# Kernel optimization log

Hardware: AMD Instinct MI355X
Metric: run time of the kernel (lower is better)

The kernel has to match this reference:

```python
import jax, jax.numpy as jnp
import numpy as np

CONF_THR = 0.01
IOU_THR = 0.45
TOPK = 200
B, N, C = 32, 32768, 81


def centroids2corners(b):
    # (..., 4) cx,cy,w,h -> xmin,ymin,xmax,ymax
    cx, cy, w, h = b[..., 0], b[..., 1], b[..., 2], b[..., 3]
    half_w, half_h = w * 0.5, h * 0.5
    return jnp.stack([cx - half_w, cy - half_h, cx + half_w, cy + half_h], axis=-1)


def iou_matrix(a, b):
    # a: (M,4), b: (N,4) corner format -> (M,N) IoU
    lt = jnp.maximum(a[:, None, :2], b[None, :, :2])
    rb = jnp.minimum(a[:, None, 2:], b[None, :, 2:])
    wh = jnp.clip(rb - lt, 0.0)
    inter = wh[..., 0] * wh[..., 1]
    area_a = (a[:, 2] - a[:, 0]) * (a[:, 3] - a[:, 1])
    area_b = (b[:, 2] - b[:, 0]) * (b[:, 3] - b[:, 1])
    return inter / (area_a[:, None] + area_b[None, :] - inter)


def nms_class(conf_c, loc, c_idx):
    # conf_c: (N,), loc: (N,4). Greedy NMS on topk highest-conf boxes above threshold.
    masked = jnp.where(conf_c > CONF_THR, conf_c, -jnp.inf)
    top_conf, idx = jax.lax.top_k(masked, TOPK)          # descending order == conf sort
    boxes = loc[idx]                                      # (TOPK, 4) centroid form
    corners = centroids2corners(boxes)
    ious = iou_matrix(corners, corners)                   # (TOPK, TOPK)
    valid = jnp.isfinite(top_conf)                        # passed conf threshold
    ar = jnp.arange(TOPK)

    def body(i, keep):
        # if box i survives, suppress later boxes with IoU > threshold
        suppress = (ious[i] > IOU_THR) & keep[i] & (ar > i)
        return keep & ~suppress

    keep = jax.lax.fori_loop(0, TOPK, body, valid)
    cls = jnp.full((TOPK, 1), c_idx, dtype=loc.dtype)
    out6 = jnp.concatenate([cls, top_conf[:, None], boxes], axis=1)  # (TOPK, 6)
    # padded slots (suppressed / below-threshold) filled with -1, mirroring the
    # original's "-1" sentinel for empty results
    return jnp.where(keep[:, None], out6, -1.0), keep


def reference(inf_cand_loc, inf_cand_conf):
    Cm1 = inf_cand_conf.shape[2] - 1  # last class is background, skipped
    cls_ids = jnp.arange(Cm1, dtype=inf_cand_loc.dtype)
    per_image = jax.vmap(nms_class, in_axes=(1, None, 0))   # over classes
    per_batch = jax.vmap(per_image, in_axes=(0, 0, None))   # over batch
    boxes, keep = per_batch(inf_cand_conf[:, :, :Cm1], inf_cand_loc, cls_ids)
    # boxes: (B, C-1, TOPK, 6=(class, conf, cx, cy, w, h)); keep: validity mask
    return boxes, keep


def setup_inputs() -> dict:
    key = jax.random.key(0)
    k1, k2 = jax.random.split(key)
    inf_cand_loc = jax.random.uniform(k1, (B, N, 4), dtype=jnp.float32)
    inf_cand_conf = jax.random.uniform(k2, (B, N, C), dtype=jnp.float32)
    return {"inf_cand_loc": inf_cand_loc, "inf_cand_conf": inf_cand_conf}
```

## Files before the change

kernel.cpp:

```cpp
#include <hip/hip_runtime.h>
#include <cstdint>

#define B_      32
#define N_      32768
#define C_      81
#define NCLS    80
#define TOPK    200
#define CONF_T  0.01f
#define IOU_T   0.45f
#define NTH     256
#define NBC     (B_ * NCLS)

#define M_IOU   0.450000017881393432617187500

#define THR_F    0.984375f
#define THR_BITS 0x3F7C0000u
#define CAP2     768

#define ANCH_PB  512
#define NCHUNK   (N_ / ANCH_PB)
#define SLAB_F4  (ANCH_PB * C_ / 4)
#define CAPB     1024

#define HBASE   129024
#define HBUCK   1024

#define SCAP    256

#define OFF_CNT   0
#define OFF_FLAGS 16384
#define OFF_CAND  32768
#define WS_NEED  (OFF_CAND + (size_t)NBC * CAP2 * 8)

#define WAVE_LGKM() asm volatile("s_waitcnt lgkmcnt(0)" ::: "memory")

__global__ void zero_hdr(int* __restrict__ p) {
    int i = blockIdx.x * blockDim.x + threadIdx.x;
    if (i < 8192) p[i] = 0;
}

__global__ __launch_bounds__(NTH) void filter_k(const float* __restrict__ conf,
                                                int* __restrict__ cnt,
                                                uint2* __restrict__ cand) {
    const int tid   = threadIdx.x;
    const int blk   = blockIdx.x;
    const int b     = blk >> 6;
    const int chunk = blk & (NCHUNK - 1);
    const uint32_t n0 = (uint32_t)chunk * ANCH_PB;
    const float4* slab = (const float4*)(conf + ((size_t)b * N_ + n0) * C_);

    __shared__ uint2 stage[CAPB];
    __shared__ int   lhist[NCLS];
    __shared__ int   lpos[NCLS];
    __shared__ int   gbase[NCLS];
    __shared__ int   ltot;

    for (int k = tid; k < NCLS; k += NTH) { lhist[k] = 0; lpos[k] = 0; }
    if (tid == 0) ltot = 0;
    __syncthreads();

    auto emit = [&](uint32_t e, float v) {
        uint32_t c = e % (uint32_t)C_;
        if (c < NCLS) {
            uint32_t nl = e / (uint32_t)C_;
            int q = atomicAdd(&ltot, 1);
            atomicAdd(&lhist[c], 1);
            if (q < CAPB)
                stage[q] = make_uint2(__float_as_uint(v), (c << 16) | nl);
        }
    };
    auto proc4 = [&](float4 x, uint32_t q) {
        if (x.x >= THR_F || x.y >= THR_F || x.z >= THR_F || x.w >= THR_F) {
            uint32_t e = q * 4u;
            if (x.x >= THR_F) emit(e + 0u, x.x);
            if (x.y >= THR_F) emit(e + 1u, x.y);
            if (x.z >= THR_F) emit(e + 2u, x.z);
            if (x.w >= THR_F) emit(e + 3u, x.w);
        }
    };

    uint32_t qb = (uint32_t)tid;
#pragma unroll 1
    for (int s = 0; s < 5; ++s, qb += 8 * NTH) {
        float4 v[8];
#pragma unroll
        for (int u = 0; u < 8; ++u) v[u] = slab[qb + u * NTH];
#pragma unroll
        for (int u = 0; u < 8; ++u) proc4(v[u], qb + u * NTH);
    }
    if (tid < SLAB_F4 - 5 * 8 * NTH) {
        uint32_t q = 5u * 8u * NTH + (uint32_t)tid;
        proc4(slab[q], q);
    }
    __syncthreads();

    const int tot = ltot;
    if (tot > CAPB) {
        for (int k = tid; k < NCLS; k += NTH)
            atomicAdd(&cnt[b * NCLS + k], CAP2 + 1);
        return;
    }
    if (tid < NCLS)
        gbase[tid] = atomicAdd(&cnt[b * NCLS + tid], lhist[tid]);
    __syncthreads();

    for (int q = tid; q < tot; q += NTH) {
        uint2 s = stage[q];
        uint32_t c  = s.y >> 16;
        uint32_t nl = s.y & 0xFFFFu;
        int pos = atomicAdd(&lpos[c], 1);
        int dst = gbase[c] + pos;
        if (dst < CAP2)
            cand[(size_t)(b * NCLS + c) * CAP2 + dst] = make_uint2(s.x, n0 + nl);
    }
}

#define TSL 10048

__global__ __launch_bounds__(NTH) void wave_select_k(const float* __restrict__ loc,
                                                     const int* __restrict__ cnt,
                                                     const uint2* __restrict__ cand,
                                                     int* __restrict__ flags,
                                                     float* __restrict__ out) {
#pragma clang fp contract(off)
    const int tid  = threadIdx.x;
    const int lane = tid & 63;
    const int wv   = tid >> 6;
    const int bc   = blockIdx.x * 4 + wv;
    const int b    = bc / NCLS;
    const int c    = bc - b * NCLS;

    __shared__ __align__(16) char smem[4 * TSL];
    char* tb = smem + wv * TSL;
    unsigned long long* surv = (unsigned long long*)tb;
    int*    keep_l = (int*)tb;
    float4* box_s  = (float4*)(tb + 2048);
    int*    hist   = (int*)(tb + 2048);
    float4* cor_s  = (float4*)(tb + 5248);
    float*  area_s = (float*)(tb + 8448);
    float*  tval   = (float*)(tb + 9248);

    const int M = cnt[bc];
    if (M < TOPK || M > CAP2) {
        if (lane == 0) flags[bc] = 1;
        return;
    }
    const unsigned long long lmask_lt = (1ull << lane) - 1ull;

    const uint2* src = cand + (size_t)bc * CAP2;
    unsigned long long key[12];
#pragma unroll
    for (int r = 0; r < 12; ++r) {
        int i = lane + 64 * r;
        uint2 s = (i < M) ? src[i] : make_uint2(0u, 0u);
        key[r] = ((unsigned long long)s.x << 32) | (uint32_t)(~s.y);
    }
    ((int4*)hist)[lane] = make_int4(0, 0, 0, 0);
    WAVE_LGKM();

#pragma unroll
    for (int r = 0; r < 12; ++r) {
        if (lane + 64 * r < M) {
            uint32_t k = ((uint32_t)(key[r] >> 32) - THR_BITS) >> 10;
            atomicAdd(&hist[k > 255u ? 255u : k], 1);
        }
    }
    WAVE_LGKM();

    int cut;
    {
        int4 h = ((const int4*)hist)[63 - lane];
        int s3 = h.w, s2 = s3 + h.z, s1 = s2 + h.y, s0 = s1 + h.x;
        int tot = s0;
#pragma unroll
        for (int d = 1; d < 64; d <<= 1) {
            int t = __shfl_up(tot, d);
            if (lane >= d) tot += t;
        }
        int before = tot - s0;
        bool hit = (before < TOPK) && (before + s0 >= TOPK);
        int mycut = 0;
        if (hit) {
            int inner = (before + s3 >= TOPK) ? 3 : (before + s2 >= TOPK) ? 2
                      : (before + s1 >= TOPK) ? 1 : 0;
            mycut = (63 - lane) * 4 + inner;
        }
        unsigned long long hm = __ballot(hit);
        cut = __shfl(mycut, __ffsll(hm) - 1);
    }
    const uint32_t edge = THR_BITS + ((uint32_t)cut << 10);

    int S = 0;
#pragma unroll
    for (int r = 0; r < 12; ++r) {
        bool take = (lane + 64 * r < M) && ((uint32_t)(key[r] >> 32) >= edge);
        unsigned long long m = __ballot(take);
        if (take) {
            int pos = S + (int)__popcll(m & lmask_lt);
            if (pos < SCAP) surv[pos] = key[r];
        }
        S += (int)__popcll(m);
    }
    if (S > SCAP) {
        if (lane == 0) flags[bc] = 1;
        return;
    }
    WAVE_LGKM();

    unsigned long long me0 = surv[lane], me1 = surv[lane + 64], me2 = surv[lane + 128];
    unsigned long long me3 = (lane + 192 < S) ? surv[lane + 192] : ~0ull;
    int r0 = 0, r1 = 0, r2 = 0, r3 = 0;
#pragma unroll 4
    for (int j = 0; j < S; ++j) {
        unsigned long long kj = surv[j];
        r0 += kj > me0; r1 += kj > me1; r2 += kj > me2; r3 += kj > me3;
    }
    const float4* loc4 = (const float4*)(loc + ((size_t)b * N_) * 4);
    auto place = [&](unsigned long long me, int rk, bool valid) {
        if (valid && rk < TOPK) {
            int idx = (int)(~(uint32_t)me);
            float4 bx = loc4[idx];
            float hw = bx.z * 0.5f;
            float hh = bx.w * 0.5f;
            float4 cr = make_float4(bx.x - hw, bx.y - hh, bx.x + hw, bx.y + hh);
            box_s[rk] = bx;
            cor_s[rk] = cr;
            area_s[rk] = (cr.z - cr.x) * (cr.w - cr.y);
            tval[rk]  = __uint_as_float((uint32_t)(me >> 32));
        }
    };
    place(me0, r0, true);
    place(me1, r1, true);
    place(me2, r2, true);
    place(me3, r3, lane + 192 < S);
    WAVE_LGKM();

    float4 d0 = cor_s[lane], d1 = cor_s[64 + lane], d2 = cor_s[128 + lane];
    float4 d3 = (lane < 8) ? cor_s[192 + lane] : d0;
    float ab0 = area_s[lane], ab1 = area_s[64 + lane], ab2 = area_s[128 + lane];
    float ab3 = (lane < 8) ? area_s[192 + lane] : 0.0f;
    unsigned long long k0 = ~0ull, k1 = ~0ull, k2 = ~0ull, k3 = (1ull << 8) - 1ull;

    auto iou_gt = [&](float4 a, float aa, float4 d, float ab) -> bool {
        float ltx = fmaxf(a.x, d.x), lty = fmaxf(a.y, d.y);
        float rbx = fminf(a.z, d.z), rby = fminf(a.w, d.w);
        float w = fmaxf(rbx - ltx, 0.0f);
        float h = fmaxf(rby - lty, 0.0f);
        float inter = w * h;
        float U = (aa + ab) - inter;
        return ((double)inter > M_IOU * (double)U);
    };

    float4 crn = cor_s[0];
    float  arn = area_s[0];
#define NMS_ROWS(W, KW, APPLY)                                            \
    for (int ii = 0; ii < 64; ++ii) {                                     \
        const int i = W * 64 + ii;                                        \
        if (i >= TOPK) break;                                             \
        float4 a = crn; float aa = arn;                                   \
        if (i + 1 < TOPK) { crn = cor_s[i + 1]; arn = area_s[i + 1]; }    \
        if ((KW >> ii) & 1ull) {                                          \
            unsigned long long gt = ~((2ull << ii) - 1ull);               \
            APPLY                                                         \
        }                                                                 \
    }
    NMS_ROWS(0, k0, {
        unsigned long long m0 = __ballot(iou_gt(a, aa, d0, ab0));
        unsigned long long m1 = __ballot(iou_gt(a, aa, d1, ab1));
        unsigned long long m2 = __ballot(iou_gt(a, aa, d2, ab2));
        unsigned long long m3 = __ballot(iou_gt(a, aa, d3, ab3));
        k0 &= ~(m0 & gt); k1 &= ~m1; k2 &= ~m2; k3 &= ~m3;
    })
    NMS_ROWS(1, k1, {
        unsigned long long m1 = __ballot(iou_gt(a, aa, d1, ab1));
        unsigned long long m2 = __ballot(iou_gt(a, aa, d2, ab2));
        unsigned long long m3 = __ballot(iou_gt(a, aa, d3, ab3));
        k1 &= ~(m1 & gt); k2 &= ~m2; k3 &= ~m3;
    })
    NMS_ROWS(2, k2, {
        unsigned long long m2 = __ballot(iou_gt(a, aa, d2, ab2));
        unsigned long long m3 = __ballot(iou_gt(a, aa, d3, ab3));
        k2 &= ~(m2 & gt); k3 &= ~m3;
    })
    NMS_ROWS(3, k3, {
        unsigned long long m3 = __ballot(iou_gt(a, aa, d3, ab3));
        k3 &= ~(m3 & gt);
    })
#undef NMS_ROWS

    keep_l[lane]       = (int)((k0 >> lane) & 1ull);
    keep_l[64 + lane]  = (int)((k1 >> lane) & 1ull);
    keep_l[128 + lane] = (int)((k2 >> lane) & 1ull);
    if (lane < 8) keep_l[192 + lane] = (int)((k3 >> lane) & 1ull);
    WAVE_LGKM();

    const float cls_f = (float)c;
    float* obase = out + (size_t)bc * (TOPK * 6);
#pragma unroll 1
    for (int t = 0; t < 19; ++t) {
        int k = lane + 64 * t;
        if (k < TOPK * 6) {
            int rk = (k * 10923) >> 16;
            int f  = k - rk * 6;
            float val;
            if (f == 0)      val = cls_f;
            else if (f == 1) val = tval[rk];
            else             val = ((const float*)box_s)[rk * 4 + (f - 2)];
            obase[k] = keep_l[rk] ? val : -1.0f;
        }
    }
    float* kbase = out + (size_t)NBC * (TOPK * 6) + (size_t)bc * TOPK;
#pragma unroll
    for (int t = 0; t < 4; ++t) {
        int rk = lane + 64 * t;
        if (rk < TOPK) kbase[rk] = keep_l[rk] ? 1.0f : 0.0f;
    }
}

#define SUPS      5
#define SM_A      0
#define SM_B      8000
#define SM_BOX    8000
#define SM_COR    11200
#define SM_TVAL   14400
#define SM_TIDX   15200
#define SM_CTRL   16000
#define SM_KEEPW  16016
#define SM_AREA   16048
#define SM_TOTAL  16848

__global__ __launch_bounds__(NTH) void rescue_k(const float* __restrict__ conf,
                                                const float* __restrict__ loc,
                                                const int* __restrict__ cnt,
                                                const uint2* __restrict__ cand,
                                                const int* __restrict__ flags,
                                                float* __restrict__ out,
                                                int use_ws) {
#pragma clang fp contract(off)
    const int bc = blockIdx.x;
    if (flags && flags[bc] == 0) return;
    const int b   = bc / NCLS;
    const int c   = bc - b * NCLS;
    const int tid = threadIdx.x;
    const int lane = tid & 63;
    const int wv   = tid >> 6;

    __shared__ __align__(16) char smem[SM_TOTAL];
    unsigned long long* surv = (unsigned long long*)(smem + SM_A);
    unsigned long long* sup  = (unsigned long long*)(smem + SM_A);
    float*  ostage = (float*)(smem + SM_A);
    int*    hist   = (int*)(smem + SM_B);
    float4* box_s  = (float4*)(smem + SM_BOX);
    float4* cor_s  = (float4*)(smem + SM_COR);
    float*  top_val = (float*)(smem + SM_TVAL);
    int*    top_idx = (int*)(smem + SM_TIDX);
    int*    ctrl   = (int*)(smem + SM_CTRL);
    unsigned long long* keepw = (unsigned long long*)(smem + SM_KEEPW);
    float*  area_s = (float*)(smem + SM_AREA);

    int M = use_ws ? cnt[bc] : 0;
    const bool fast = use_ws && (M >= TOPK) && (M <= CAP2);
    int S = 0;

    if (fast) {
        const uint2* src = cand + (size_t)bc * CAP2;
        uint2 my0 = make_uint2(0u, 0u), my1 = make_uint2(0u, 0u), my2 = make_uint2(0u, 0u);
        if (tid           < M) my0 = src[tid];
        if (tid +     NTH < M) my1 = src[tid + NTH];
        if (tid + 2 * NTH < M) my2 = src[tid + 2 * NTH];
        hist[tid] = 0;
        if (tid == 0) ctrl[2] = 0;
        __syncthreads();
        if (tid           < M) { uint32_t k = (my0.x - THR_BITS) >> 10; atomicAdd(&hist[k > 255u ? 255u : k], 1); }
        if (tid +     NTH < M) { uint32_t k = (my1.x - THR_BITS) >> 10; atomicAdd(&hist[k > 255u ? 255u : k], 1); }
        if (tid + 2 * NTH < M) { uint32_t k = (my2.x - THR_BITS) >> 10; atomicAdd(&hist[k > 255u ? 255u : k], 1); }
        __syncthreads();
        if (tid < 64) {
            int4 h = ((const int4*)hist)[63 - tid];
            int s3 = h.w, s2 = s3 + h.z, s1 = s2 + h.y, s0 = s1 + h.x;
            int tot = s0;
#pragma unroll
            for (int d = 1; d < 64; d <<= 1) {
                int t = __shfl_up(tot, d);
                if (tid >= d) tot += t;
            }
            int before = tot - s0;
            if (before < TOPK && before + s0 >= TOPK) {
                int inner = (before + s3 >= TOPK) ? 3 : (before + s2 >= TOPK) ? 2
                          : (before + s1 >= TOPK) ? 1 : 0;
                ctrl[1] = (63 - tid) * 4 + inner;
            }
        }
        __syncthreads();
        if (tid < TOPK) {
            top_idx[tid] = -1;
            area_s[tid] = 0.0f;
            box_s[tid] = make_float4(-1.f, -1.f, -1.f, -1.f);
            cor_s[tid] = make_float4(0.f, 0.f, 0.f, 0.f);
        }
        const uint32_t edge = THR_BITS + ((uint32_t)ctrl[1] << 10);
#define COMPACT(MY)                                                          \
        {                                                                    \
            bool take = (MY.x >= edge);                                      \
            unsigned long long mask = __ballot(take);                        \
            int base = 0;                                                    \
            if (lane == 0 && mask) base = atomicAdd(&ctrl[2], (int)__popcll(mask)); \
            base = __shfl(base, 0);                                          \
            if (take) {                                                      \
                int pos = base + (int)__popcll(mask & ((1ull << lane) - 1ull)); \
                if (pos < CAP2)                                              \
                    surv[pos] = ((unsigned long long)MY.x << 32) | (uint32_t)(~MY.y); \
            }                                                                \
        }
        COMPACT(my0) COMPACT(my1) COMPACT(my2)
#undef COMPACT
        __syncthreads();
        S = min(ctrl[2], CAP2);
    } else {
        for (int k = tid; k < HBUCK; k += NTH) hist[k] = 0;
        if (tid == 0) ctrl[2] = 0;
        __syncthreads();
        const float* col = conf + ((size_t)b * N_) * C_ + c;
        for (int n = tid; n < N_; n += NTH) {
            float v = col[(size_t)n * C_];
            if (v >= 0.5f) {
                int bkt = (int)(__float_as_uint(v) >> 13) - HBASE;
                atomicAdd(&hist[min(bkt, HBUCK - 1)], 1);
            }
        }
        __syncthreads();
        if (tid == 0) {
            int acc = 0, cut = -1;
            for (int k = HBUCK - 1; k >= 0; --k) {
                acc += hist[k];
                if (acc >= TOPK) { cut = k; break; }
            }
            ctrl[1] = cut;
        }
        __syncthreads();
        const int   cutv = ctrl[1];
        const float vcut = (cutv >= 0) ? __uint_as_float((uint32_t)(HBASE + cutv) << 13)
                                       : CONF_T;
        for (int n = tid; n < N_; n += NTH) {
            float v = col[(size_t)n * C_];
            bool take = (cutv >= 0) ? (v >= vcut) : (v > CONF_T);
            if (take) {
                int p = atomicAdd(&ctrl[2], 1);
                if (p < CAP2)
                    surv[p] = ((unsigned long long)__float_as_uint(v) << 32)
                            | (uint32_t)(~(uint32_t)n);
            }
        }
        __syncthreads();
        if (tid < TOPK) {
            top_idx[tid] = -1;
            area_s[tid] = 0.0f;
            box_s[tid] = make_float4(-1.f, -1.f, -1.f, -1.f);
            cor_s[tid] = make_float4(0.f, 0.f, 0.f, 0.f);
        }
        S = min(ctrl[2], CAP2);
        __syncthreads();
    }

    for (int i = tid; i < S; i += NTH) {
        unsigned long long me = surv[i];
        int rank = 0;
#pragma unroll 4
        for (int j = 0; j < S; ++j)
            rank += (surv[j] > me);
        if (rank < TOPK) {
            int idx = (int)(~(uint32_t)me);
            top_val[rank] = __uint_as_float((uint32_t)(me >> 32));
            top_idx[rank] = idx;
            float4 bx = *(const float4*)(loc + ((size_t)b * N_ + (size_t)idx) * 4);
            float hw = bx.z * 0.5f;
            float hh = bx.w * 0.5f;
            float4 cr = make_float4(bx.x - hw, bx.y - hh, bx.x + hw, bx.y + hh);
            box_s[rank] = bx;
            cor_s[rank] = cr;
            area_s[rank] = (cr.z - cr.x) * (cr.w - cr.y);
        }
    }
    __syncthreads();

    {
        bool v = (tid < TOPK) && (top_idx[tid] >= 0);
        unsigned long long m = __ballot(v);
        if (lane == 0) keepw[wv] = m;
    }

    {
        const int j = tid;
        float4 d = make_float4(0.f, 0.f, 0.f, 0.f);
        float  areaB = 0.0f;
        const bool jv = (j < TOPK);
        if (jv) { d = cor_s[j]; areaB = area_s[j]; }
#pragma unroll 2
        for (int i = 0; i < TOPK; ++i) {
            float4 a = cor_s[i];
            bool s = false;
            if (jv && j > i) {
                float ltx = fmaxf(a.x, d.x), lty = fmaxf(a.y, d.y);
                float rbx = fminf(a.z, d.z), rby = fminf(a.w, d.w);
                float w  = fmaxf(rbx - ltx, 0.0f);
                float h  = fmaxf(rby - lty, 0.0f);
                float inter = w * h;
                float U = (area_s[i] + areaB) - inter;
                s = ((double)inter > M_IOU * (double)U);
            }
            unsigned long long m = __ballot(s);
            if (lane == 0) sup[i * SUPS + wv] = m;
        }
    }
    __syncthreads();

    if (tid < 64) {
        unsigned long long r0[4], r1[4], r2[4], r3[4];
#pragma unroll
        for (int w = 0; w < 4; ++w) {
            r0[w] = sup[(0 * 64 + tid) * SUPS + w];
            r1[w] = sup[(1 * 64 + tid) * SUPS + w];
            r2[w] = sup[(2 * 64 + tid) * SUPS + w];
            r3[w] = (192 + tid < TOPK) ? sup[(192 + tid) * SUPS + w] : 0ull;
        }
        unsigned long long k0 = keepw[0], k1 = keepw[1], k2 = keepw[2], k3 = keepw[3];
#define GREEDY_BLK(KW, RR)                                            \
        for (int ii = 0; ii < 64; ++ii) {                             \
            if ((KW >> ii) & 1ull) {                                  \
                k0 &= ~__shfl(RR[0], ii);                             \
                k1 &= ~__shfl(RR[1], ii);                             \
                k2 &= ~__shfl(RR[2], ii);                             \
                k3 &= ~__shfl(RR[3], ii);                             \
            }                                                         \
        }
        GREEDY_BLK(k0, r0)
        GREEDY_BLK(k1, r1)
        GREEDY_BLK(k2, r2)
        GREEDY_BLK(k3, r3)
#undef GREEDY_BLK
        if (tid == 0) { keepw[0] = k0; keepw[1] = k1; keepw[2] = k2; keepw[3] = k3; }
    }
    __syncthreads();

    if (tid < TOPK) {
        const bool kp = (keepw[tid >> 6] >> (tid & 63)) & 1ull;
        float4 bx = box_s[tid];
        float* o = ostage + tid * 6;
        if (kp) {
            o[0] = (float)c;   o[1] = top_val[tid];
            o[2] = bx.x; o[3] = bx.y; o[4] = bx.z; o[5] = bx.w;
        } else {
            o[0] = -1.f; o[1] = -1.f; o[2] = -1.f;
            o[3] = -1.f; o[4] = -1.f; o[5] = -1.f;
        }
        out[(size_t)NBC * TOPK * 6 + (size_t)bc * TOPK + tid] = kp ? 1.0f : 0.0f;
    }
    __syncthreads();
    {
        float4* dst = (float4*)(out + (size_t)bc * TOPK * 6);
        const float4* src4 = (const float4*)ostage;
        for (int k = tid; k < TOPK * 6 / 4; k += NTH) dst[k] = src4[k];
    }
}

extern "C" void kernel_launch(void* const* d_in, const int* in_sizes, int n_in,
                              void* d_out, int out_size, void* d_ws, size_t ws_size,
                              hipStream_t stream) {
    (void)in_sizes; (void)n_in; (void)out_size;
    const float* loc  = (const float*)d_in[0];
    const float* conf = (const float*)d_in[1];
    float* out = (float*)d_out;

    const bool use_ws = (d_ws != nullptr) && (ws_size >= WS_NEED);
    int*   cnt   = (int*)((char*)d_ws + OFF_CNT);
    int*   flags = (int*)((char*)d_ws + OFF_FLAGS);
    uint2* cand  = (uint2*)((char*)d_ws + OFF_CAND);

    if (use_ws) {
        hipLaunchKernelGGL(zero_hdr, dim3(32), dim3(NTH), 0, stream, cnt);
        hipLaunchKernelGGL(filter_k, dim3(B_ * NCHUNK), dim3(NTH), 0, stream,
                           conf, cnt, cand);
        hipLaunchKernelGGL(wave_select_k, dim3(NBC / 4), dim3(NTH), 0, stream,
                           loc, cnt, cand, flags, out);
        hipLaunchKernelGGL(rescue_k, dim3(NBC), dim3(NTH), 0, stream,
                           conf, loc, cnt, cand, flags, out, 1);
    } else {
        hipLaunchKernelGGL(rescue_k, dim3(NBC), dim3(NTH), 0, stream,
                           conf, loc, (const int*)nullptr, (const uint2*)nullptr,
                           (const int*)nullptr, out, 0);
    }
}
```

Baseline: 144.4 us.

## Queue fallback classes into compact worklist and shrink rescue grid

The fast wave kernel now appends failing (batch,class) ids to a global work queue via an atomic instead of setting per-slot flags, and the rescue kernel runs a persistent 64-block grid that loops only over queued items rather than launching 2560 blocks that mostly exit. Candidates are stored pre-packed as 64-bit sort keys so the wave kernel loads them directly, the rank loop reads two keys per LDS load, and output boxes are re-gathered from global loc only for kept entries, staged in LDS and written as float4. The rescue path loses its cached-candidate fast branch and always recomputes from conf, and a large queue would be serialized over only 64 blocks.

```diff
diff --git a/kernel.cpp b/kernel.cpp
--- a/kernel.cpp
+++ b/kernel.cpp
@@ -28,7 +28,8 @@
 #define SCAP    256
 
 #define OFF_CNT   0
-#define OFF_FLAGS 16384
+#define OFF_QN    12288
+#define OFF_QBUF  16384
 #define OFF_CAND  32768
 #define WS_NEED  (OFF_CAND + (size_t)NBC * CAP2 * 8)
 
@@ -36,7 +37,7 @@
 
 __global__ void zero_hdr(int* __restrict__ p) {
     int i = blockIdx.x * blockDim.x + threadIdx.x;
-    if (i < 8192) p[i] = 0;
+    if (i < 4096) p[i] = 0;
 }
 
 __global__ __launch_bounds__(NTH) void filter_k(const float* __restrict__ conf,
@@ -111,16 +112,17 @@
         int pos = atomicAdd(&lpos[c], 1);
         int dst = gbase[c] + pos;
         if (dst < CAP2)
-            cand[(size_t)(b * NCLS + c) * CAP2 + dst] = make_uint2(s.x, n0 + nl);
+            cand[(size_t)(b * NCLS + c) * CAP2 + dst] = make_uint2(~(n0 + nl), s.x);
     }
 }
 
-#define TSL 10048
+#define TSL 7648
 
 __global__ __launch_bounds__(NTH) void wave_select_k(const float* __restrict__ loc,
                                                      const int* __restrict__ cnt,
-                                                     const uint2* __restrict__ cand,
-                                                     int* __restrict__ flags,
+                                                     const unsigned long long* __restrict__ cand,
+                                                     int* __restrict__ qn,
+                                                     int* __restrict__ qbuf,
                                                      float* __restrict__ out) {
 #pragma clang fp contract(off)
     const int tid  = threadIdx.x;
@@ -133,27 +135,26 @@
     __shared__ __align__(16) char smem[4 * TSL];
     char* tb = smem + wv * TSL;
     unsigned long long* surv = (unsigned long long*)tb;
-    int*    keep_l = (int*)tb;
-    float4* box_s  = (float4*)(tb + 2048);
+    float*  ostage = (float*)tb;
+    float4* cor_s  = (float4*)(tb + 2048);
     int*    hist   = (int*)(tb + 2048);
-    float4* cor_s  = (float4*)(tb + 5248);
-    float*  area_s = (float*)(tb + 8448);
-    float*  tval   = (float*)(tb + 9248);
+    float*  area_s = (float*)(tb + 5248);
+    float*  tval   = (float*)(tb + 6048);
+    int*    tidx   = (int*)(tb + 6848);
 
     const int M = cnt[bc];
     if (M < TOPK || M > CAP2) {
-        if (lane == 0) flags[bc] = 1;
+        if (lane == 0) { int p = atomicAdd(qn, 1); qbuf[p] = bc; }
         return;
     }
     const unsigned long long lmask_lt = (1ull << lane) - 1ull;
 
-    const uint2* src = cand + (size_t)bc * CAP2;
+    const unsigned long long* src = cand + (size_t)bc * CAP2;
     unsigned long long key[12];
 #pragma unroll
     for (int r = 0; r < 12; ++r) {
         int i = lane + 64 * r;
-        uint2 s = (i < M) ? src[i] : make_uint2(0u, 0u);
-        key[r] = ((unsigned long long)s.x << 32) | (uint32_t)(~s.y);
+        key[r] = (i < M) ? src[i] : 0ull;
     }
     ((int4*)hist)[lane] = make_int4(0, 0, 0, 0);
     WAVE_LGKM();
@@ -202,7 +203,7 @@
         S += (int)__popcll(m);
     }
     if (S > SCAP) {
-        if (lane == 0) flags[bc] = 1;
+        if (lane == 0) { int p = atomicAdd(qn, 1); qbuf[p] = bc; }
         return;
     }
     WAVE_LGKM();
@@ -210,10 +211,21 @@
     unsigned long long me0 = surv[lane], me1 = surv[lane + 64], me2 = surv[lane + 128];
     unsigned long long me3 = (lane + 192 < S) ? surv[lane + 192] : ~0ull;
     int r0 = 0, r1 = 0, r2 = 0, r3 = 0;
-#pragma unroll 4
-    for (int j = 0; j < S; ++j) {
-        unsigned long long kj = surv[j];
-        r0 += kj > me0; r1 += kj > me1; r2 += kj > me2; r3 += kj > me3;
+    {
+        const ulonglong2* sv2 = (const ulonglong2*)surv;
+        const int Sh = S >> 1;
+#pragma unroll 2
+        for (int j2 = 0; j2 < Sh; ++j2) {
+            ulonglong2 kj = sv2[j2];
+            r0 += (kj.x > me0) + (kj.y > me0);
+            r1 += (kj.x > me1) + (kj.y > me1);
+            r2 += (kj.x > me2) + (kj.y > me2);
+            r3 += (kj.x > me3) + (kj.y > me3);
+        }
+        if (S & 1) {
+            unsigned long long kj = surv[S - 1];
+            r0 += kj > me0; r1 += kj > me1; r2 += kj > me2; r3 += kj > me3;
+        }
     }
     const float4* loc4 = (const float4*)(loc + ((size_t)b * N_) * 4);
     auto place = [&](unsigned long long me, int rk, bool valid) {
@@ -223,10 +235,10 @@
             float hw = bx.z * 0.5f;
             float hh = bx.w * 0.5f;
             float4 cr = make_float4(bx.x - hw, bx.y - hh, bx.x + hw, bx.y + hh);
-            box_s[rk] = bx;
             cor_s[rk] = cr;
             area_s[rk] = (cr.z - cr.x) * (cr.w - cr.y);
-            tval[rk]  = __uint_as_float((uint32_t)(me >> 32));
+            tval[rk] = __uint_as_float((uint32_t)(me >> 32));
+            tidx[rk] = idx;
         }
     };
     place(me0, r0, true);
@@ -288,32 +300,32 @@
     })
 #undef NMS_ROWS
 
-    keep_l[lane]       = (int)((k0 >> lane) & 1ull);
-    keep_l[64 + lane]  = (int)((k1 >> lane) & 1ull);
-    keep_l[128 + lane] = (int)((k2 >> lane) & 1ull);
-    if (lane < 8) keep_l[192 + lane] = (int)((k3 >> lane) & 1ull);
-    WAVE_LGKM();
-
     const float cls_f = (float)c;
-    float* obase = out + (size_t)bc * (TOPK * 6);
-#pragma unroll 1
-    for (int t = 0; t < 19; ++t) {
-        int k = lane + 64 * t;
-        if (k < TOPK * 6) {
-            int rk = (k * 10923) >> 16;
-            int f  = k - rk * 6;
-            float val;
-            if (f == 0)      val = cls_f;
-            else if (f == 1) val = tval[rk];
-            else             val = ((const float*)box_s)[rk * 4 + (f - 2)];
-            obase[k] = keep_l[rk] ? val : -1.0f;
-        }
-    }
     float* kbase = out + (size_t)NBC * (TOPK * 6) + (size_t)bc * TOPK;
 #pragma unroll
     for (int t = 0; t < 4; ++t) {
         int rk = lane + 64 * t;
-        if (rk < TOPK) kbase[rk] = keep_l[rk] ? 1.0f : 0.0f;
+        if (rk < TOPK) {
+            unsigned long long kw = (t == 0) ? k0 : (t == 1) ? k1 : (t == 2) ? k2 : k3;
+            bool kp = (kw >> lane) & 1ull;
+            float4 bx = make_float4(-1.f, -1.f, -1.f, -1.f);
+            float tv = -1.f, cf = -1.f;
+            if (kp) { bx = loc4[tidx[rk]]; tv = tval[rk]; cf = cls_f; }
+            float* o = ostage + rk * 6;
+            o[0] = cf;   o[1] = tv;
+            o[2] = bx.x; o[3] = bx.y; o[4] = bx.z; o[5] = bx.w;
+            kbase[rk] = kp ? 1.0f : 0.0f;
+        }
+    }
+    WAVE_LGKM();
+    {
+        float4* dst = (float4*)(out + (size_t)bc * (TOPK * 6));
+        const float4* s4 = (const float4*)ostage;
+#pragma unroll
+        for (int t = 0; t < 5; ++t) {
+            int k = lane + 64 * t;
+            if (k < TOPK * 6 / 4) dst[k] = s4[k];
+        }
     }
 }
 
@@ -331,19 +343,15 @@
 
 __global__ __launch_bounds__(NTH) void rescue_k(const float* __restrict__ conf,
                                                 const float* __restrict__ loc,
-                                                const int* __restrict__ cnt,
-                                                const uint2* __restrict__ cand,
-                                                const int* __restrict__ flags,
+                                                const int* __restrict__ qn,
+                                                const int* __restrict__ qbuf,
                                                 float* __restrict__ out,
-                                                int use_ws) {
+                                                int qmode) {
 #pragma clang fp contract(off)
-    const int bc = blockIdx.x;
-    if (flags && flags[bc] == 0) return;
-    const int b   = bc / NCLS;
-    const int c   = bc - b * NCLS;
-    const int tid = threadIdx.x;
+    const int tid  = threadIdx.x;
     const int lane = tid & 63;
     const int wv   = tid >> 6;
+    const int niter = qmode ? *qn : NBC;
 
     __shared__ __align__(16) char smem[SM_TOTAL];
     unsigned long long* surv = (unsigned long long*)(smem + SM_A);
@@ -358,65 +366,11 @@
     unsigned long long* keepw = (unsigned long long*)(smem + SM_KEEPW);
     float*  area_s = (float*)(smem + SM_AREA);
 
-    int M = use_ws ? cnt[bc] : 0;
-    const bool fast = use_ws && (M >= TOPK) && (M <= CAP2);
-    int S = 0;
-
-    if (fast) {
-        const uint2* src = cand + (size_t)bc * CAP2;
-        uint2 my0 = make_uint2(0u, 0u), my1 = make_uint2(0u, 0u), my2 = make_uint2(0u, 0u);
-        if (tid           < M) my0 = src[tid];
-        if (tid +     NTH < M) my1 = src[tid + NTH];
-        if (tid + 2 * NTH < M) my2 = src[tid + 2 * NTH];
-        hist[tid] = 0;
-        if (tid == 0) ctrl[2] = 0;
-        __syncthreads();
-        if (tid           < M) { uint32_t k = (my0.x - THR_BITS) >> 10; atomicAdd(&hist[k > 255u ? 255u : k], 1); }
-        if (tid +     NTH < M) { uint32_t k = (my1.x - THR_BITS) >> 10; atomicAdd(&hist[k > 255u ? 255u : k], 1); }
-        if (tid + 2 * NTH < M) { uint32_t k = (my2.x - THR_BITS) >> 10; atomicAdd(&hist[k > 255u ? 255u : k], 1); }
-        __syncthreads();
-        if (tid < 64) {
-            int4 h = ((const int4*)hist)[63 - tid];
-            int s3 = h.w, s2 = s3 + h.z, s1 = s2 + h.y, s0 = s1 + h.x;
-            int tot = s0;
-#pragma unroll
-            for (int d = 1; d < 64; d <<= 1) {
-                int t = __shfl_up(tot, d);
-                if (tid >= d) tot += t;
-            }
-            int before = tot - s0;
-            if (before < TOPK && before + s0 >= TOPK) {
-                int inner = (before + s3 >= TOPK) ? 3 : (before + s2 >= TOPK) ? 2
-                          : (before + s1 >= TOPK) ? 1 : 0;
-                ctrl[1] = (63 - tid) * 4 + inner;
-            }
-        }
-        __syncthreads();
-        if (tid < TOPK) {
-            top_idx[tid] = -1;
-            area_s[tid] = 0.0f;
-            box_s[tid] = make_float4(-1.f, -1.f, -1.f, -1.f);
-            cor_s[tid] = make_float4(0.f, 0.f, 0.f, 0.f);
-        }
-        const uint32_t edge = THR_BITS + ((uint32_t)ctrl[1] << 10);
-#define COMPACT(MY)                                                          \
-        {                                                                    \
-            bool take = (MY.x >= edge);                                      \
-            unsigned long long mask = __ballot(take);                        \
-            int base = 0;                                                    \
-            if (lane == 0 && mask) base = atomicAdd(&ctrl[2], (int)__popcll(mask)); \
-            base = __shfl(base, 0);                                          \
-            if (take) {                                                      \
-                int pos = base + (int)__popcll(mask & ((1ull << lane) - 1ull)); \
-                if (pos < CAP2)                                              \
-                    surv[pos] = ((unsigned long long)MY.x << 32) | (uint32_t)(~MY.y); \
-            }                                                                \
-        }
-        COMPACT(my0) COMPACT(my1) COMPACT(my2)
-#undef COMPACT
-        __syncthreads();
-        S = min(ctrl[2], CAP2);
-    } else {
+    for (int qi = blockIdx.x; qi < niter; qi += gridDim.x) {
+        const int bc = qmode ? qbuf[qi] : qi;
+        const int b  = bc / NCLS;
+        const int c  = bc - b * NCLS;
+
         for (int k = tid; k < HBUCK; k += NTH) hist[k] = 0;
         if (tid == 0) ctrl[2] = 0;
         __syncthreads();
@@ -458,108 +412,109 @@
             box_s[tid] = make_float4(-1.f, -1.f, -1.f, -1.f);
             cor_s[tid] = make_float4(0.f, 0.f, 0.f, 0.f);
         }
-        S = min(ctrl[2], CAP2);
-        __syncthreads();
-    }
-
-    for (int i = tid; i < S; i += NTH) {
-        unsigned long long me = surv[i];
-        int rank = 0;
+        const int S = min(ctrl[2], CAP2);
+        __syncthreads();
+
+        for (int i = tid; i < S; i += NTH) {
+            unsigned long long me = surv[i];
+            int rank = 0;
 #pragma unroll 4
-        for (int j = 0; j < S; ++j)
-            rank += (surv[j] > me);
-        if (rank < TOPK) {
-            int idx = (int)(~(uint32_t)me);
-            top_val[rank] = __uint_as_float((uint32_t)(me >> 32));
-            top_idx[rank] = idx;
-            float4 bx = *(const float4*)(loc + ((size_t)b * N_ + (size_t)idx) * 4);
-            float hw = bx.z * 0.5f;
-            float hh = bx.w * 0.5f;
-            float4 cr = make_float4(bx.x - hw, bx.y - hh, bx.x + hw, bx.y + hh);
-            box_s[rank] = bx;
-            cor_s[rank] = cr;
-            area_s[rank] = (cr.z - cr.x) * (cr.w - cr.y);
-        }
-    }
-    __syncthreads();
-
-    {
-        bool v = (tid < TOPK) && (top_idx[tid] >= 0);
-        unsigned long long m = __ballot(v);
-        if (lane == 0) keepw[wv] = m;
-    }
-
-    {
-        const int j = tid;
-        float4 d = make_float4(0.f, 0.f, 0.f, 0.f);
-        float  areaB = 0.0f;
-        const bool jv = (j < TOPK);
-        if (jv) { d = cor_s[j]; areaB = area_s[j]; }
+            for (int j = 0; j < S; ++j)
+                rank += (surv[j] > me);
+            if (rank < TOPK) {
+                int idx = (int)(~(uint32_t)me);
+                top_val[rank] = __uint_as_float((uint32_t)(me >> 32));
+                top_idx[rank] = idx;
+                float4 bx = *(const float4*)(loc + ((size_t)b * N_ + (size_t)idx) * 4);
+                float hw = bx.z * 0.5f;
+                float hh = bx.w * 0.5f;
+                float4 cr = make_float4(bx.x - hw, bx.y - hh, bx.x + hw, bx.y + hh);
+                box_s[rank] = bx;
+                cor_s[rank] = cr;
+                area_s[rank] = (cr.z - cr.x) * (cr.w - cr.y);
+            }
+        }
+        __syncthreads();
+
+        {
+            bool v = (tid < TOPK) && (top_idx[tid] >= 0);
+            unsigned long long m = __ballot(v);
+            if (lane == 0) keepw[wv] = m;
+        }
+
+        {
+            const int j = tid;
+            float4 d = make_float4(0.f, 0.f, 0.f, 0.f);
+            float  areaB = 0.0f;
+            const bool jv = (j < TOPK);
+            if (jv) { d = cor_s[j]; areaB = area_s[j]; }
 #pragma unroll 2
-        for (int i = 0; i < TOPK; ++i) {
-            float4 a = cor_s[i];
-            bool s = false;
-            if (jv && j > i) {
-                float ltx = fmaxf(a.x, d.x), lty = fmaxf(a.y, d.y);
-                float rbx = fminf(a.z, d.z), rby = fminf(a.w, d.w);
-                float w  = fmaxf(rbx - ltx, 0.0f);
-                float h  = fmaxf(rby - lty, 0.0f);
-                float inter = w * h;
-                float U = (area_s[i] + areaB) - inter;
-                s = ((double)inter > M_IOU * (double)U);
-            }
-            unsigned long long m = __ballot(s);
-            if (lane == 0) sup[i * SUPS + wv] = m;
-        }
-    }
-    __syncthreads();
-
-    if (tid < 64) {
-        unsigned long long r0[4], r1[4], r2[4], r3[4];
-#pragma unroll
-        for (int w = 0; w < 4; ++w) {
-            r0[w] = sup[(0 * 64 + tid) * SUPS + w];
-            r1[w] = sup[(1 * 64 + tid) * SUPS + w];
-            r2[w] = sup[(2 * 64 + tid) * SUPS + w];
-            r3[w] = (192 + tid < TOPK) ? sup[(192 + tid) * SUPS + w] : 0ull;
-        }
-        unsigned long long k0 = keepw[0], k1 = keepw[1], k2 = keepw[2], k3 = keepw[3];
+            for (int i = 0; i < TOPK; ++i) {
+                float4 a = cor_s[i];
+                bool s = false;
+                if (jv && j > i && top_idx[j] >= 0) {
+                    float ltx = fmaxf(a.x, d.x), lty = fmaxf(a.y, d.y);
+                    float rbx = fminf(a.z, d.z), rby = fminf(a.w, d.w);
+                    float w  = fmaxf(rbx - ltx, 0.0f);
+                    float h  = fmaxf(rby - lty, 0.0f);
+                    float inter = w * h;
+                    float U = (area_s[i] + areaB) - inter;
+                    s = ((double)inter > M_IOU * (double)U);
+                }
+                unsigned long long m = __ballot(s);
+                if (lane == 0) sup[i * SUPS + wv] = m;
+            }
+        }
+        __syncthreads();
+
+        if (tid < 64) {
+            unsigned long long r0[4], r1[4], r2[4], r3[4];
+#pragma unroll
+            for (int w = 0; w < 4; ++w) {
+                r0[w] = sup[(0 * 64 + tid) * SUPS + w];
+                r1[w] = sup[(1 * 64 + tid) * SUPS + w];
+                r2[w] = sup[(2 * 64 + tid) * SUPS + w];
+                r3[w] = (192 + tid < TOPK) ? sup[(192 + tid) * SUPS + w] : 0ull;
+            }
+            unsigned long long k0 = keepw[0], k1 = keepw[1], k2 = keepw[2], k3 = keepw[3];
 #define GREEDY_BLK(KW, RR)                                            \
-        for (int ii = 0; ii < 64; ++ii) {                             \
-            if ((KW >> ii) & 1ull) {                                  \
-                k0 &= ~__shfl(RR[0], ii);                             \
-                k1 &= ~__shfl(RR[1], ii);                             \
-                k2 &= ~__shfl(RR[2], ii);                             \
-                k3 &= ~__shfl(RR[3], ii);                             \
-            }                                                         \
-        }
-        GREEDY_BLK(k0, r0)
-        GREEDY_BLK(k1, r1)
-        GREEDY_BLK(k2, r2)
-        GREEDY_BLK(k3, r3)
+            for (int ii = 0; ii < 64; ++ii) {                         \
+                if ((KW >> ii) & 1ull) {                              \
+                    k0 &= ~__shfl(RR[0], ii);                         \
+                    k1 &= ~__shfl(RR[1], ii);                         \
+                    k2 &= ~__shfl(RR[2], ii);                         \
+                    k3 &= ~__shfl(RR[3], ii);                         \
+                }                                                     \
+            }
+            GREEDY_BLK(k0, r0)
+            GREEDY_BLK(k1, r1)
+            GREEDY_BLK(k2, r2)
+            GREEDY_BLK(k3, r3)
 #undef GREEDY_BLK
-        if (tid == 0) { keepw[0] = k0; keepw[1] = k1; keepw[2] = k2; keepw[3] = k3; }
-    }
-    __syncthreads();
-
-    if (tid < TOPK) {
-        const bool kp = (keepw[tid >> 6] >> (tid & 63)) & 1ull;
-        float4 bx = box_s[tid];
-        float* o = ostage + tid * 6;
-        if (kp) {
-            o[0] = (float)c;   o[1] = top_val[tid];
-            o[2] = bx.x; o[3] = bx.y; o[4] = bx.z; o[5] = bx.w;
-        } else {
-            o[0] = -1.f; o[1] = -1.f; o[2] = -1.f;
-            o[3] = -1.f; o[4] = -1.f; o[5] = -1.f;
-        }
-        out[(size_t)NBC * TOPK * 6 + (size_t)bc * TOPK + tid] = kp ? 1.0f : 0.0f;
-    }
-    __syncthreads();
-    {
-        float4* dst = (float4*)(out + (size_t)bc * TOPK * 6);
-        const float4* src4 = (const float4*)ostage;
-        for (int k = tid; k < TOPK * 6 / 4; k += NTH) dst[k] = src4[k];
+            if (tid == 0) { keepw[0] = k0; keepw[1] = k1; keepw[2] = k2; keepw[3] = k3; }
+        }
+        __syncthreads();
+
+        if (tid < TOPK) {
+            const bool kp = (keepw[tid >> 6] >> (tid & 63)) & 1ull;
+            float4 bx = box_s[tid];
+            float* o = ostage + tid * 6;
+            if (kp) {
+                o[0] = (float)c;   o[1] = top_val[tid];
+                o[2] = bx.x; o[3] = bx.y; o[4] = bx.z; o[5] = bx.w;
+            } else {
+                o[0] = -1.f; o[1] = -1.f; o[2] = -1.f;
+                o[3] = -1.f; o[4] = -1.f; o[5] = -1.f;
+            }
+            out[(size_t)NBC * TOPK * 6 + (size_t)bc * TOPK + tid] = kp ? 1.0f : 0.0f;
+        }
+        __syncthreads();
+        {
+            float4* dst = (float4*)(out + (size_t)bc * TOPK * 6);
+            const float4* src4 = (const float4*)ostage;
+            for (int k = tid; k < TOPK * 6 / 4; k += NTH) dst[k] = src4[k];
+        }
+        __syncthreads();
     }
 }
 
@@ -572,21 +527,22 @@
     float* out = (float*)d_out;
 
     const bool use_ws = (d_ws != nullptr) && (ws_size >= WS_NEED);
-    int*   cnt   = (int*)((char*)d_ws + OFF_CNT);
-    int*   flags = (int*)((char*)d_ws + OFF_FLAGS);
-    uint2* cand  = (uint2*)((char*)d_ws + OFF_CAND);
+    int*   cnt  = (int*)((char*)d_ws + OFF_CNT);
+    int*   qn   = (int*)((char*)d_ws + OFF_QN);
+    int*   qbuf = (int*)((char*)d_ws + OFF_QBUF);
+    uint2* cand = (uint2*)((char*)d_ws + OFF_CAND);
 
     if (use_ws) {
-        hipLaunchKernelGGL(zero_hdr, dim3(32), dim3(NTH), 0, stream, cnt);
+        hipLaunchKernelGGL(zero_hdr, dim3(16), dim3(NTH), 0, stream, cnt);
         hipLaunchKernelGGL(filter_k, dim3(B_ * NCHUNK), dim3(NTH), 0, stream,
                            conf, cnt, cand);
         hipLaunchKernelGGL(wave_select_k, dim3(NBC / 4), dim3(NTH), 0, stream,
-                           loc, cnt, cand, flags, out);
-        hipLaunchKernelGGL(rescue_k, dim3(NBC), dim3(NTH), 0, stream,
-                           conf, loc, cnt, cand, flags, out, 1);
+                           loc, cnt, (const unsigned long long*)cand, qn, qbuf, out);
+        hipLaunchKernelGGL(rescue_k, dim3(64), dim3(NTH), 0, stream,
+                           conf, loc, qn, qbuf, out, 1);
     } else {
         hipLaunchKernelGGL(rescue_k, dim3(NBC), dim3(NTH), 0, stream,
-                           conf, loc, (const int*)nullptr, (const uint2*)nullptr,
-                           (const int*)nullptr, out, 0);
+                           conf, loc, (const int*)nullptr, (const int*)nullptr,
+                           out, 0);
     }
 }
```

After: 140.0 us. -3.0%, faster.
